# Kernel optimization log

Measured on AMD Instinct MI355X. Metric: run time of the kernel, lower is better.

## Reference

```python
import jax, jax.numpy as jnp
import numpy as np

DEL_ID, STOP_ID, PAD_ID, KEEP_ID = 3, 5, 0, 2


def lstm(x, h0, c0, Wi, Wh, bi, bh):
    """Single-layer batch-first LSTM, PyTorch gate order (i,f,g,o).
    x: [B,T,E]; h0,c0: [B,H]. Returns (ys [B,T,H], h [B,H], c [B,H])."""
    b = bi + bh

    def step(carry, xt):
        h, c = carry
        g = xt @ Wi.T + h @ Wh.T + b  # [B,4H]
        i, f, gg, o = jnp.split(g, 4, axis=-1)
        c = jax.nn.sigmoid(f) * c + jax.nn.sigmoid(i) * jnp.tanh(gg)
        h = jax.nn.sigmoid(o) * jnp.tanh(c)
        return (h, c), h

    (h, c), ys = jax.lax.scan(step, (h0, c0), jnp.swapaxes(x, 0, 1))
    return jnp.swapaxes(ys, 0, 1), h, c


def setup_inputs() -> dict:
    key = jax.random.key(0)
    ks = jax.random.split(key, 20)
    B, T, S, H, E, V = 32, 100, 100, 512, 256, 30000
    s = 0.02
    inp = {
        "input_edits": jax.random.randint(ks[0], (B, T), 0, V),
        "simp_sent": jax.random.randint(ks[1], (B, S), 0, V),
        "org_ids": jax.random.randint(ks[2], (B, S), 0, V),
        "encoder_outputs_org": jax.random.normal(ks[3], (B, S, H), dtype=jnp.float32),
        "h0": jnp.zeros((B, H), jnp.float32),
        "c0": jnp.zeros((B, H), jnp.float32),
        "emb": jax.random.normal(ks[4], (V, E), dtype=jnp.float32) * s,
        "Wi_e": jax.random.normal(ks[5], (4 * H, E), dtype=jnp.float32) * s,
        "Wh_e": jax.random.normal(ks[6], (4 * H, H), dtype=jnp.float32) * s,
        "bi_e": jnp.zeros((4 * H,), jnp.float32),
        "bh_e": jnp.zeros((4 * H,), jnp.float32),
        "Wi_w": jax.random.normal(ks[7], (4 * H, E), dtype=jnp.float32) * s,
        "Wh_w": jax.random.normal(ks[8], (4 * H, H), dtype=jnp.float32) * s,
        "bi_w": jnp.zeros((4 * H,), jnp.float32),
        "bh_w": jnp.zeros((4 * H,), jnp.float32),
        "Wp": jax.random.normal(ks[9], (H, H), dtype=jnp.float32) * s,
        "Wm": jax.random.normal(ks[10], (E, 4 * H), dtype=jnp.float32) * s,
        "bm": jnp.zeros((E,), jnp.float32),
        "b_out": jnp.zeros((30000,), jnp.float32),
    }
    return inp


def reference(input_edits, simp_sent, org_ids, encoder_outputs_org, h0, c0,
              emb, Wi_e, Wh_e, bi_e, bh_e, Wi_w, Wh_w, bi_w, bh_w,
              Wp, Wm, bm, b_out):
    # teacher_forcing_ratio = 1.0 -> teacher-forcing branch only
    B, T = input_edits.shape
    S = encoder_outputs_org.shape[1]
    Sw = simp_sent.shape[1]

    # run both LSTMs over the full teacher-forced sequences
    out_e, he, ce = lstm(emb[input_edits], h0, c0, Wi_e, Wh_e, bi_e, bh_e)  # [B,T,H]
    out_w, _, _ = lstm(emb[simp_sent], h0, c0, Wi_w, Wh_w, bi_w, bh_w)      # [B,Sw,H]

    # attention over encoder outputs
    key_org = out_e @ Wp.T                                                   # [B,T,H]
    attn = jax.nn.softmax(jnp.einsum('bth,bsh->bts', key_org, encoder_outputs_org), axis=-1)
    applied = jnp.einsum('bts,bsh->bth', attn, encoder_outputs_org)          # [B,T,H]

    # counters are exclusive cumsums of gold-action masks over input_edits[:,1:]
    a = input_edits[:, 1:]                                                   # gold actions, [B,T-1]
    inc_del = ((a == KEEP_ID) | (a == DEL_ID)).astype(jnp.int32)
    inc_ins = ((a != DEL_ID) & (a != STOP_ID) & (a != PAD_ID)).astype(jnp.int32)
    ctr_del = jnp.clip(jnp.cumsum(inc_del, 1) - inc_del, 0, S - 1)           # [B,T-1]
    ctr_ins = jnp.clip(jnp.cumsum(inc_ins, 1) - inc_ins, 0, Sw - 1)

    H = encoder_outputs_org.shape[2]
    c = jnp.take_along_axis(encoder_outputs_org,
                            jnp.broadcast_to(ctr_del[:, :, None], (B, T - 1, H)), axis=1)
    c_word = jnp.take_along_axis(out_w,
                                 jnp.broadcast_to(ctr_ins[:, :, None], (B, T - 1, H)), axis=1)

    feat = jnp.concatenate([out_e[:, :T - 1], applied[:, :T - 1], c, c_word], axis=-1)  # [B,T-1,4H]
    hmlp = jnp.tanh(feat @ Wm.T + bm)                                        # [B,T-1,E]
    logp = jax.nn.log_softmax(hmlp @ emb.T + b_out, axis=-1)                 # [B,T-1,V]
    return logp, he[None], ce[None]
```

## Files before the change

kernel.cpp:

```cpp
#include <hip/hip_runtime.h>
#include <math.h>


typedef __attribute__((ext_vector_type(8))) short short8v;
typedef __attribute__((ext_vector_type(4))) float f32x4;
typedef unsigned long long ull;

#define LSTM_BLOCKS 64
#define NTIL 235

__device__ __forceinline__ float sigf(float x){ return 1.0f/(1.0f + __expf(-x)); }
__device__ __forceinline__ float tanhc(float x){
  x = fminf(fmaxf(x, -15.f), 15.f);
  float e = __expf(2.f*x);
  return (e-1.f)/(e+1.f);
}
__device__ __forceinline__ short f2bf(float f){
  unsigned u = __float_as_uint(f);
  u = (u + 0x7fffu + ((u >> 16) & 1u)) >> 16;
  return (short)u;
}
__device__ __forceinline__ float bf2f(short s){
  return __uint_as_float(((unsigned)(unsigned short)s) << 16);
}

__global__ void prep_permute(
    const float* __restrict__ Wi_e, const float* __restrict__ Wh_e,
    const float* __restrict__ bi_e, const float* __restrict__ bh_e,
    const float* __restrict__ Wi_w, const float* __restrict__ Wh_w,
    const float* __restrict__ bi_w, const float* __restrict__ bh_w,
    short* __restrict__ WiPh_e, short* __restrict__ WhPh_e, float* __restrict__ biasP_e,
    short* __restrict__ WiPh_w, short* __restrict__ WhPh_w, float* __restrict__ biasP_w)
{
  const int z = blockIdx.y;
  const float* Wi = z ? Wi_w : Wi_e;
  const float* Wh = z ? Wh_w : Wh_e;
  const float* bi = z ? bi_w : bi_e;
  const float* bh = z ? bh_w : bh_e;
  short* WiPh = z ? WiPh_w : WiPh_e;
  short* WhPh = z ? WhPh_w : WhPh_e;
  float* biasP = z ? biasP_w : biasP_e;

  int idx = blockIdx.x*256 + threadIdx.x;
  {
    int op = idx >> 9, k = idx & 511;
    int u = op >> 2, g = op & 3;
    WhPh[idx] = f2bf(Wh[(g*512+u)*512 + k]);
  }
  if (idx < 2048*256) {
    int op = idx >> 8, e = idx & 255;
    int u = op >> 2, g = op & 3;
    WiPh[idx] = f2bf(Wi[(g*512+u)*256 + e]);
  }
  if (idx < 2048) {
    int u = idx >> 2, g = idx & 3;
    biasP[idx] = bi[g*512+u] + bh[g*512+u];
  }
}

__global__ void misc_prep(const float* __restrict__ emb,
                          const float* __restrict__ Wp, const float* __restrict__ Wm,
                          const float* __restrict__ h0, const int* __restrict__ ie,
                          short* __restrict__ embh,
                          short* __restrict__ Wph, short* __restrict__ Wmh,
                          ull* __restrict__ hq, unsigned* __restrict__ bar,
                          int* __restrict__ ctr_del, int* __restrict__ ctr_ins)
{
  int idx = blockIdx.x*256 + threadIdx.x;
  if (idx < 1920000) {
    float4 v = *(const float4*)(emb + (long)idx*4);
    short4 o; o.x=f2bf(v.x); o.y=f2bf(v.y); o.z=f2bf(v.z); o.w=f2bf(v.w);
    *(short4*)(embh + (long)idx*4) = o;
  } else if (idx < 1985536) {
    int i = idx - 1920000;
    float4 v = *(const float4*)(Wp + (long)i*4);
    short4 o; o.x=f2bf(v.x); o.y=f2bf(v.y); o.z=f2bf(v.z); o.w=f2bf(v.w);
    *(short4*)(Wph + (long)i*4) = o;
  } else if (idx < 2116608) {
    int i = idx - 1985536;
    float4 v = *(const float4*)(Wm + (long)i*4);
    short4 o; o.x=f2bf(v.x); o.y=f2bf(v.y); o.z=f2bf(v.z); o.w=f2bf(v.w);
    *(short4*)(Wmh + (long)i*4) = o;
  } else if (idx < 2124800) {
    int i = idx - 2116608;
    int b = (i >> 7) & 31, q = i & 127;
    const float* src = h0 + b*512 + q*4;
    ull v = ((ull)(unsigned short)f2bf(src[3]) << 48) |
            ((ull)(unsigned short)f2bf(src[2]) << 32) |
            ((ull)(unsigned short)f2bf(src[1]) << 16) |
            ((ull)(unsigned short)f2bf(src[0]));
    hq[i] = v;
  } else if (idx < 2124928) {
    bar[idx - 2124800] = 0u;
  } else if (idx < 2124960) {
    int b = idx - 2124928;
    int rd = 0, ri = 0;
    for (int t = 0; t < 99; ++t) {
      int a = ie[b*100 + t + 1];
      int incd = (a == 2 || a == 3) ? 1 : 0;
      int inci = (a != 3 && a != 5 && a != 0) ? 1 : 0;
      ctr_del[b*99 + t] = min(rd, 99);
      ctr_ins[b*99 + t] = min(ri, 99);
      rd += incd; ri += inci;
    }
  }
}

__global__ __launch_bounds__(256) void enc_prep(const float* __restrict__ enc,
                                                short* __restrict__ ench,
                                                short* __restrict__ encTh)
{
  __shared__ short tile[100][72];
  const int b = blockIdx.x;
  const float* src = enc + (long)b*51200;
  short* de = ench  + (long)b*51200;
  short* dt = encTh + (long)b*65536;
  const int tid = threadIdx.x;
  for (int c = 0; c < 8; ++c) {
    #pragma unroll
    for (int i = 0; i < 25; ++i) {
      int idx = tid + 256*i;
      int k = idx >> 6, j = idx & 63;
      short h = f2bf(src[(long)k*512 + c*64 + j]);
      tile[k][j] = h;
      de[(long)k*512 + c*64 + j] = h;
    }
    __syncthreads();
    #pragma unroll
    for (int i = 0; i < 32; ++i) {
      int idx = tid + 256*i;
      int n = idx >> 7, kk = idx & 127;
      dt[(long)(c*64 + n)*128 + kk] = (kk < 100) ? tile[kk][n] : (short)0;
    }
    __syncthreads();
  }
}

template<int GATHER,int CVT_A,int BIAS,int TANH,int OUT_BF16>
__device__ __forceinline__ void gemm_mfma_body(
    const void* __restrict__ Av, const int* __restrict__ tok,
    const short* __restrict__ Bh, const float* __restrict__ bias,
    void* __restrict__ Cv, int M, int N, int K, int lda, int ldc,
    int bxk, int byk)
{
  __shared__ short As[128][72];
  __shared__ short Bs[128][72];
  const int bm = bxk * 128;
  const int bn = byk * 128;
  const int tid = threadIdx.x;
  const int w = tid >> 6, l = tid & 63;
  const int wr = (w >> 1) * 64, wc = (w & 1) * 64;
  const int lr = l & 15, kg = l >> 4;

  f32x4 acc[4][4] = {};

  for (int k0 = 0; k0 < K; k0 += 64) {
    #pragma unroll
    for (int q = 0; q < 4; ++q) {
      int ci = tid + 256*q;
      int r = ci >> 3, ch = ci & 7;
      int ar = bm + r; if (ar > M-1) ar = M-1;
      if (GATHER) ar = tok[ar];
      if (CVT_A) {
        const float* ap = ((const float*)Av) + (long)ar*lda + k0 + ch*8;
        float4 v0 = *(const float4*)ap;
        float4 v1 = *(const float4*)(ap + 4);
        short8v s;
        s[0]=f2bf(v0.x); s[1]=f2bf(v0.y); s[2]=f2bf(v0.z); s[3]=f2bf(v0.w);
        s[4]=f2bf(v1.x); s[5]=f2bf(v1.y); s[6]=f2bf(v1.z); s[7]=f2bf(v1.w);
        *(short8v*)&As[r][ch*8] = s;
      } else {
        *(short8v*)&As[r][ch*8] =
            *(const short8v*)(((const short*)Av) + (long)ar*lda + k0 + ch*8);
      }
      int br = bn + r; if (br > N-1) br = N-1;
      *(short8v*)&Bs[r][ch*8] = *(const short8v*)(Bh + (long)br*K + k0 + ch*8);
    }
    __syncthreads();
    #pragma unroll
    for (int ks = 0; ks < 2; ++ks) {
      short8v a[4], b[4];
      #pragma unroll
      for (int m = 0; m < 4; ++m)
        a[m] = *(const short8v*)&As[wr + m*16 + lr][ks*32 + kg*8];
      #pragma unroll
      for (int n = 0; n < 4; ++n)
        b[n] = *(const short8v*)&Bs[wc + n*16 + lr][ks*32 + kg*8];
      #pragma unroll
      for (int m = 0; m < 4; ++m)
        #pragma unroll
        for (int n = 0; n < 4; ++n)
          acc[m][n] = __builtin_amdgcn_mfma_f32_16x16x32_bf16(a[m], b[n], acc[m][n], 0, 0, 0);
    }
    __syncthreads();
  }

  #pragma unroll
  for (int n = 0; n < 4; ++n) {
    int col = bn + wc + n*16 + lr;
    bool cok = (col < N);
    float bv = (BIAS && cok) ? bias[col] : 0.f;
    #pragma unroll
    for (int m = 0; m < 4; ++m) {
      int row0 = bm + wr + m*16 + kg*4;
      #pragma unroll
      for (int r = 0; r < 4; ++r) {
        int row = row0 + r;
        if (cok && row < M) {
          float v = acc[m][n][r] + bv;
          if (TANH) v = tanhc(v);
          if (OUT_BF16) ((short*)Cv)[(long)row*ldc + col] = f2bf(v);
          else          ((float*)Cv)[(long)row*ldc + col] = v;
        }
      }
    }
  }
}

template<int GATHER,int CVT_A,int BIAS,int TANH,int OUT_BF16>
__global__ __launch_bounds__(256) void gemm_mfma(
    const void* __restrict__ Av, const int* __restrict__ tok,
    const short* __restrict__ Bh, const float* __restrict__ bias,
    void* __restrict__ Cv, int M, int N, int K, int lda, int ldc)
{
  gemm_mfma_body<GATHER,CVT_A,BIAS,TANH,OUT_BF16>(
      Av, tok, Bh, bias, Cv, M, N, K, lda, ldc, blockIdx.x, blockIdx.y);
}

template<int BIAS,int TANH,int OUT_BF16>
__global__ __launch_bounds__(256) void gemm_mfma_bat(
    const short* __restrict__ Ah, const short* __restrict__ Bh,
    const float* __restrict__ bias, void* __restrict__ Cv,
    int M, int N, int K, int lda, int ldc, long sA, long sB, long sC)
{
  const int z = blockIdx.z;
  void* C2 = OUT_BF16 ? (void*)((short*)Cv + (long)z*sC)
                      : (void*)((float*)Cv + (long)z*sC);
  gemm_mfma_body<0,0,BIAS,TANH,OUT_BF16>(
      (const void*)(Ah + (long)z*sA), nullptr, Bh + (long)z*sB, bias,
      C2, M, N, K, lda, ldc, blockIdx.x, blockIdx.y);
}

__global__ __launch_bounds__(256) void xproj_mfma(
    const float* __restrict__ emb,
    const int* __restrict__ tokA, const int* __restrict__ tokB,
    const short* __restrict__ WA, const short* __restrict__ WB,
    const float* __restrict__ bA, const float* __restrict__ bB,
    short* __restrict__ outA, short* __restrict__ outB)
{
  const int z = blockIdx.z;
  gemm_mfma_body<1,1,1,0,1>(
      emb, z ? tokB : tokA, z ? WB : WA, z ? bB : bA,
      z ? (void*)outB : (void*)outA, 3200, 2048, 256, 256, 2048,
      blockIdx.x, blockIdx.y);
}

__global__ __launch_bounds__(256) void logits_mfma_partial(
    const short* __restrict__ Ah,
    const short* __restrict__ Bh,
    const float* __restrict__ bias,
    short* __restrict__ Cg,
    float2* __restrict__ partial)
{
  __shared__ short As[128][72];
  __shared__ short Bs[128][72];
  __shared__ float2 red[128][2];
  const int bm = blockIdx.x * 128;
  const int bn = blockIdx.y * 128;
  const int tid = threadIdx.x;
  const int w = tid >> 6, l = tid & 63;
  const int wr = (w >> 1) * 64, wc = (w & 1) * 64;
  const int lr = l & 15, kg = l >> 4;

  f32x4 acc[4][4] = {};

  #pragma unroll
  for (int k0 = 0; k0 < 256; k0 += 64) {
    #pragma unroll
    for (int q = 0; q < 4; ++q) {
      int ci = tid + 256*q;
      int r = ci >> 3, ch = ci & 7;
      int ar = bm + r; if (ar > 3167) ar = 3167;
      *(short8v*)&As[r][ch*8] = *(const short8v*)(Ah + (long)ar*256 + k0 + ch*8);
      int br = bn + r; if (br > 29999) br = 29999;
      *(short8v*)&Bs[r][ch*8] = *(const short8v*)(Bh + (long)br*256 + k0 + ch*8);
    }
    __syncthreads();
    #pragma unroll
    for (int ks = 0; ks < 2; ++ks) {
      short8v a[4], b[4];
      #pragma unroll
      for (int m = 0; m < 4; ++m)
        a[m] = *(const short8v*)&As[wr + m*16 + lr][ks*32 + kg*8];
      #pragma unroll
      for (int n = 0; n < 4; ++n)
        b[n] = *(const short8v*)&Bs[wc + n*16 + lr][ks*32 + kg*8];
      #pragma unroll
      for (int m = 0; m < 4; ++m)
        #pragma unroll
        for (int n = 0; n < 4; ++n)
          acc[m][n] = __builtin_amdgcn_mfma_f32_16x16x32_bf16(a[m], b[n], acc[m][n], 0, 0, 0);
    }
    __syncthreads();
  }

  #pragma unroll
  for (int n = 0; n < 4; ++n) {
    int col = bn + wc + n*16 + lr;
    float bv = (col < 30000) ? bias[col] : 0.f;
    #pragma unroll
    for (int m = 0; m < 4; ++m)
      #pragma unroll
      for (int r = 0; r < 4; ++r)
        acc[m][n][r] = (col < 30000) ? acc[m][n][r] + bv : -INFINITY;
  }
  #pragma unroll
  for (int m = 0; m < 4; ++m) {
    #pragma unroll
    for (int r = 0; r < 4; ++r) {
      float a0 = acc[m][0][r], a1 = acc[m][1][r], a2 = acc[m][2][r], a3 = acc[m][3][r];
      float mx = fmaxf(fmaxf(a0, a1), fmaxf(a2, a3));
      #pragma unroll
      for (int off = 1; off < 16; off <<= 1) mx = fmaxf(mx, __shfl_xor(mx, off));
      float se = 0.f;
      if (mx > -INFINITY)
        se = __expf(a0-mx) + __expf(a1-mx) + __expf(a2-mx) + __expf(a3-mx);
      #pragma unroll
      for (int off = 1; off < 16; off <<= 1) se += __shfl_xor(se, off);
      if (lr == 0) red[wr + m*16 + kg*4 + r][w & 1] = make_float2(mx, se);
    }
  }
  #pragma unroll
  for (int n = 0; n < 4; ++n) {
    int col = bn + wc + n*16 + lr;
    if (col < 30000) {
      #pragma unroll
      for (int m = 0; m < 4; ++m) {
        int row0 = bm + wr + m*16 + kg*4;
        #pragma unroll
        for (int r = 0; r < 4; ++r) {
          int row = row0 + r;
          if (row < 3168) Cg[(long)row*30000 + col] = f2bf(acc[m][n][r]);
        }
      }
    }
  }
  __syncthreads();
  if (tid < 128) {
    int row = bm + tid;
    if (row < 3168) {
      float2 A = red[tid][0], B = red[tid][1];
      float M = fmaxf(A.x, B.x);
      float S = 0.f;
      if (M > -INFINITY) S = A.y*__expf(A.x - M) + B.y*__expf(B.x - M);
      partial[(long)row*NTIL + blockIdx.y] = make_float2(M, S);
    }
  }
}

__global__ __launch_bounds__(256) void sub_lse_fused(
    const short* __restrict__ Cg, const float2* __restrict__ partial,
    float* __restrict__ out)
{
  int row = blockIdx.x;
  int tid = threadIdx.x;
  float m = -INFINITY, s = 0.f;
  if (tid < NTIL) {
    float2 p = partial[(long)row*NTIL + tid];
    m = p.x; s = p.y;
  }
  #pragma unroll
  for (int off = 32; off; off >>= 1) {
    float om = __shfl_xor(m, off);
    float os = __shfl_xor(s, off);
    float nm = fmaxf(m, om);
    if (nm > -INFINITY) {
      s = s*__expf(m - nm) + os*__expf(om - nm);
      m = nm;
    }
  }
  __shared__ float sm[4], ss[4], lsh;
  int wv = tid >> 6;
  if ((tid & 63) == 0) { sm[wv] = m; ss[wv] = s; }
  __syncthreads();
  if (tid == 0) {
    float M = sm[0], S = ss[0];
    #pragma unroll
    for (int i = 1; i < 4; ++i) {
      float nm = fmaxf(M, sm[i]);
      S = S*__expf(M - nm) + ss[i]*__expf(sm[i] - nm);
      M = nm;
    }
    lsh = M + __logf(S);
  }
  __syncthreads();
  float lv = lsh;
  const short* src = Cg + (long)row*30000;
  float* dst = out + (long)row*30000;
  for (int i = tid; i < 3750; i += 256) {
    short8v v = *(const short8v*)(src + i*8);
    float4 o0, o1;
    o0.x = bf2f(v[0]) - lv; o0.y = bf2f(v[1]) - lv;
    o0.z = bf2f(v[2]) - lv; o0.w = bf2f(v[3]) - lv;
    o1.x = bf2f(v[4]) - lv; o1.y = bf2f(v[5]) - lv;
    o1.z = bf2f(v[6]) - lv; o1.w = bf2f(v[7]) - lv;
    *(float4*)(dst + i*8)     = o0;
    *(float4*)(dst + i*8 + 4) = o1;
  }
}

__global__ __launch_bounds__(256, 1) void lstm_persist(
    const short* __restrict__ WhPh_e, const short* __restrict__ WhPh_w,
    const short* __restrict__ Xp_e, const short* __restrict__ Xp_w,
    const float* __restrict__ c0_in,
    ull* __restrict__ hq,
    short* __restrict__ outT,
    float* __restrict__ out_hc,
    unsigned* __restrict__ flags)
{
  const int bx = blockIdx.x;
  const int l = bx >> 5;
  const int ublk = bx & 31;
  const int tid = threadIdx.x;
  const int w = tid >> 6, lane = tid & 63;
  const int uloc = lane >> 4;
  const int bn = lane & 15;
  const int u_global = ublk*16 + w*4 + uloc;
  const int ob = (ublk*16 + w*4) * 4;
  const int qcol = ublk*4 + w;

  const short* WhPh = l ? WhPh_w : WhPh_e;
  const short* Xp   = l ? Xp_w   : Xp_e;
  const unsigned* myfl = flags + l*32;

  __shared__ short hT[32][520];

  __hip_atomic_load(&flags[100], __ATOMIC_ACQUIRE, __HIP_MEMORY_SCOPE_AGENT);

  short8v afr[16];
  {
    const short* wp = WhPh + (long)(ob + bn)*512 + uloc*8;
    #pragma unroll
    for (int ks = 0; ks < 16; ++ks)
      afr[ks] = *(const short8v*)(wp + ks*32);
  }
  float c_s0 = c0_in[bn*512 + u_global];
  float c_s1 = c0_in[(bn+16)*512 + u_global];

  for (int t = 0; t < 100; ++t) {
    ull xq0 = *(const ull*)(Xp + ((long)(bn*100 + t))*2048 + u_global*4);
    ull xq1 = *(const ull*)(Xp + ((long)((bn+16)*100 + t))*2048 + u_global*4);
    if (t) {
      int ok;
      do {
        unsigned f = (lane < 32)
          ? __hip_atomic_load(&myfl[lane], __ATOMIC_RELAXED, __HIP_MEMORY_SCOPE_AGENT)
          : 0xffffffffu;
        ok = __all((int)(f >= (unsigned)t));
        if (!ok) __builtin_amdgcn_s_sleep(1);
      } while (!ok);
    }
    {
      const ull* hsrc = hq + (size_t)t*8192 + (l << 12);
      #pragma unroll
      for (int i = 0; i < 16; ++i) {
        int idx = tid + 256*i;
        int b = idx >> 7, q = idx & 127;
        *(ull*)&hT[b][q*4] = hsrc[idx];
      }
    }
    __syncthreads();
    f32x4 acc0 = {}, acc1 = {};
    #pragma unroll
    for (int ks = 0; ks < 16; ++ks) {
      short8v b0 = *(const short8v*)&hT[bn][ks*32 + uloc*8];
      short8v b1 = *(const short8v*)&hT[bn+16][ks*32 + uloc*8];
      acc0 = __builtin_amdgcn_mfma_f32_16x16x32_bf16(afr[ks], b0, acc0, 0, 0, 0);
      acc1 = __builtin_amdgcn_mfma_f32_16x16x32_bf16(afr[ks], b1, acc1, 0, 0, 0);
    }
    float gi = acc0[0] + bf2f((short)(xq0 & 0xffffu));
    float gf = acc0[1] + bf2f((short)((xq0 >> 16) & 0xffffu));
    float gg = acc0[2] + bf2f((short)((xq0 >> 32) & 0xffffu));
    float go = acc0[3] + bf2f((short)((xq0 >> 48) & 0xffffu));
    c_s0 = sigf(gf)*c_s0 + sigf(gi)*tanhc(gg);
    float hv0 = sigf(go)*tanhc(c_s0);
    gi = acc1[0] + bf2f((short)(xq1 & 0xffffu));
    gf = acc1[1] + bf2f((short)((xq1 >> 16) & 0xffffu));
    gg = acc1[2] + bf2f((short)((xq1 >> 32) & 0xffffu));
    go = acc1[3] + bf2f((short)((xq1 >> 48) & 0xffffu));
    c_s1 = sigf(gf)*c_s1 + sigf(gi)*tanhc(gg);
    float hv1 = sigf(go)*tanhc(c_s1);

    short hb0 = f2bf(hv0), hb1 = f2bf(hv1);
    unsigned p0 = (unsigned)(unsigned short)hb0;
    unsigned p1 = (unsigned)(unsigned short)hb1;
    unsigned a1 = __shfl_down((int)p0, 16), a2 = __shfl_down((int)p0, 32), a3 = __shfl_down((int)p0, 48);
    unsigned e1 = __shfl_down((int)p1, 16), e2 = __shfl_down((int)p1, 32), e3 = __shfl_down((int)p1, 48);
    if (uloc == 0) {
      ull q0 = ((ull)((a2 & 0xffffu) | (a3 << 16)) << 32) | ((p0 & 0xffffu) | (a1 << 16));
      ull q1 = ((ull)((e2 & 0xffffu) | (e3 << 16)) << 32) | ((p1 & 0xffffu) | (e1 << 16));
      ull* hd = hq + (size_t)(t+1)*8192 + (l << 12);
      __hip_atomic_store(&hd[(bn << 7) + qcol],      q0, __ATOMIC_RELAXED, __HIP_MEMORY_SCOPE_AGENT);
      __hip_atomic_store(&hd[((bn+16) << 7) + qcol], q1, __ATOMIC_RELAXED, __HIP_MEMORY_SCOPE_AGENT);
    }
    if (t < 99) {
      asm volatile("s_waitcnt vmcnt(0)" ::: "memory");
      __syncthreads();
      if (tid == 0)
        __hip_atomic_store(&flags[bx], (unsigned)(t+1),
                           __ATOMIC_RELAXED, __HIP_MEMORY_SCOPE_AGENT);
    }
    short* od = outT + ((long)(l*100 + t)*512 + u_global)*32;
    od[bn]    = hb0;
    od[bn+16] = hb1;
    if (t == 99 && l == 0) {
      out_hc[bn*512 + u_global]              = hv0;
      out_hc[(bn+16)*512 + u_global]         = hv1;
      out_hc[16384 + bn*512 + u_global]      = c_s0;
      out_hc[16384 + (bn+16)*512 + u_global] = c_s1;
    }
  }
}

__global__ __launch_bounds__(256) void transpose_out(
    const short* __restrict__ outT, short* __restrict__ out_e, short* __restrict__ out_w)
{
  __shared__ short tile[512][40];
  const int t = blockIdx.x, l = blockIdx.y;
  const short* src = outT + (long)(l*100 + t)*16384;
  const int tid = threadIdx.x;
  #pragma unroll
  for (int i = 0; i < 8; ++i) {
    int fi = tid + 256*i;
    int u = fi >> 2, b8 = (fi & 3)*8;
    *(short8v*)&tile[u][b8] = *(const short8v*)(src + fi*8);
  }
  __syncthreads();
  short* dst = l ? out_w : out_e;
  for (int b = 0; b < 32; ++b) {
    short* drow = dst + (long)(b*100 + t)*512;
    drow[tid]     = tile[tid][b];
    drow[tid+256] = tile[tid+256][b];
  }
}

__global__ void softmax_rows(const float* __restrict__ P, short* __restrict__ Ph)
{
  int row  = blockIdx.x*4 + (threadIdx.x >> 6);
  int lane = threadIdx.x & 63;
  const float* p = P + (long)row*128;
  short* q = Ph + (long)row*128;
  float x0 = p[lane];
  float x1 = (lane + 64 < 100) ? p[lane+64] : -INFINITY;
  float m = fmaxf(x0, x1);
  #pragma unroll
  for (int off = 32; off; off >>= 1) m = fmaxf(m, __shfl_xor(m, off));
  float e0 = __expf(x0 - m);
  float e1 = (lane + 64 < 100) ? __expf(x1 - m) : 0.f;
  float s = e0 + e1;
  #pragma unroll
  for (int off = 32; off; off >>= 1) s += __shfl_xor(s, off);
  float inv = 1.f / s;
  q[lane]      = f2bf(e0 * inv);
  q[lane + 64] = (lane + 64 < 100) ? f2bf(e1 * inv) : (short)0;
}

__global__ void feat_kernel(const short* __restrict__ out_e, const short* __restrict__ appliedh,
                            const short* __restrict__ ench, const short* __restrict__ out_w,
                            const int* __restrict__ ctr_del, const int* __restrict__ ctr_ins,
                            short* __restrict__ feat)
{
  int n = blockIdx.x;
  int b = n / 99, t = n % 99;
  int tid = threadIdx.x;
  int seg = tid >> 6;
  int off = (tid & 63) * 8;
  const short* s = (seg == 0) ? out_e    + (long)(b*100 + t)*512
                 : (seg == 1) ? appliedh + (long)(b*100 + t)*512
                 : (seg == 2) ? ench     + (long)(b*100 + ctr_del[n])*512
                              : out_w    + (long)(b*100 + ctr_ins[n])*512;
  *(short8v*)(feat + (long)n*2048 + seg*512 + off) = *(const short8v*)(s + off);
}

extern "C" void kernel_launch(void* const* d_in, const int* in_sizes, int n_in,
                              void* d_out, int out_size, void* d_ws, size_t ws_size,
                              hipStream_t stream)
{
  const int*   input_edits = (const int*)  d_in[0];
  const int*   simp_sent   = (const int*)  d_in[1];
  const float* enc   = (const float*)d_in[3];
  const float* h0    = (const float*)d_in[4];
  const float* c0    = (const float*)d_in[5];
  const float* emb   = (const float*)d_in[6];
  const float* Wi_e  = (const float*)d_in[7];
  const float* Wh_e  = (const float*)d_in[8];
  const float* bi_e  = (const float*)d_in[9];
  const float* bh_e  = (const float*)d_in[10];
  const float* Wi_w  = (const float*)d_in[11];
  const float* Wh_w  = (const float*)d_in[12];
  const float* bi_w  = (const float*)d_in[13];
  const float* bh_w  = (const float*)d_in[14];
  const float* Wp    = (const float*)d_in[15];
  const float* Wm    = (const float*)d_in[16];
  const float* bmv   = (const float*)d_in[17];
  const float* b_out = (const float*)d_in[18];
  float* out = (float*)d_out;

  float* ws = (float*)d_ws;
  size_t off = 0;
  auto alloc = [&](size_t n){ float* p = ws + off; off += (n + 63) & ~(size_t)63; return p; };

  short* WiPh_e   = (short*)alloc(262144);
  short* WiPh_w   = (short*)alloc(262144);
  float* biasP_e  = alloc(2048);
  float* biasP_w  = alloc(2048);
  short* WhPh_e   = (short*)alloc(524288);
  short* WhPh_w   = (short*)alloc(524288);
  short* Xp_e     = (short*)alloc(3276800);
  short* Xp_w     = (short*)alloc(3276800);
  short* outT     = (short*)alloc(1638400);
  short* out_e    = (short*)alloc(819200);
  short* out_w    = (short*)alloc(819200);
  ull*   hq       = (ull*)alloc(101*8192*2);
  unsigned* bar   = (unsigned*)alloc(128);
  float* Pbuf     = alloc(409600);
  short* Pbh      = (short*)alloc(204800);
  int*   ctr_del  = (int*)alloc(3168);
  int*   ctr_ins  = (int*)alloc(3168);
  short* Wph      = (short*)alloc(131072);
  short* Wmh      = (short*)alloc(262144);
  short* keyh     = (short*)alloc(819200);
  short* appliedh = (short*)alloc(819200);
  short* ench     = (short*)alloc(819200);
  short* encTh    = (short*)alloc(1048576);
  short* embh     = (short*)alloc(3840000);
  short* logith   = (short*)alloc(47520000);
  float2* partial = (float2*)alloc(3168*NTIL*2);
  short* feath    = (short*)Xp_e;
  short* hmlph    = (short*)Xp_w;

  prep_permute<<<dim3(4096,2), 256, 0, stream>>>(
      Wi_e, Wh_e, bi_e, bh_e, Wi_w, Wh_w, bi_w, bh_w,
      WiPh_e, WhPh_e, biasP_e, WiPh_w, WhPh_w, biasP_w);
  misc_prep<<<8301, 256, 0, stream>>>(emb, Wp, Wm, h0, input_edits,
                                      embh, Wph, Wmh, hq, bar, ctr_del, ctr_ins);
  enc_prep<<<32, 256, 0, stream>>>(enc, ench, encTh);

  xproj_mfma<<<dim3(25,16,2), 256, 0, stream>>>(
      emb, input_edits, simp_sent, WiPh_e, WiPh_w, biasP_e, biasP_w, Xp_e, Xp_w);

  lstm_persist<<<LSTM_BLOCKS, 256, 0, stream>>>(
      WhPh_e, WhPh_w, Xp_e, Xp_w, c0, hq, outT, out + 95040000L, bar);

  transpose_out<<<dim3(100,2), 256, 0, stream>>>(outT, out_e, out_w);

  gemm_mfma<0,0,0,0,1><<<dim3(25,4), 256, 0, stream>>>(
      out_e, nullptr, Wph, nullptr, keyh, 3200, 512, 512, 512, 512);

  gemm_mfma_bat<0,0,0><<<dim3(1,1,32), 256, 0, stream>>>(
      keyh, ench, nullptr, Pbuf, 100, 100, 512, 512, 128,
      51200, 51200, 12800);
  softmax_rows<<<800, 256, 0, stream>>>(Pbuf, Pbh);
  gemm_mfma_bat<0,0,1><<<dim3(1,4,32), 256, 0, stream>>>(
      Pbh, encTh, nullptr, appliedh, 100, 512, 128, 128, 512,
      12800, 65536, 51200);

  feat_kernel<<<3168, 256, 0, stream>>>(out_e, appliedh, ench, out_w,
                                        ctr_del, ctr_ins, feath);
  gemm_mfma<0,0,1,1,1><<<dim3(25,2), 256, 0, stream>>>(
      feath, nullptr, Wmh, bmv, hmlph, 3168, 256, 2048, 2048, 256);

  logits_mfma_partial<<<dim3(25, NTIL), 256, 0, stream>>>(
      hmlph, embh, b_out, logith, partial);
  sub_lse_fused<<<3168, 256, 0, stream>>>(logith, partial, out);
}
```

Baseline: 1.056 ms.

## Use per-wave padded flags in LSTM and derive outputs from hq history

Result: no change. 1.076 ms (+1.9%).

```diff
diff --git a/kernel.cpp b/kernel.cpp
--- a/kernel.cpp
+++ b/kernel.cpp
@@ -63,7 +63,7 @@
                           const float* __restrict__ h0, const int* __restrict__ ie,
                           short* __restrict__ embh,
                           short* __restrict__ Wph, short* __restrict__ Wmh,
-                          ull* __restrict__ hq, unsigned* __restrict__ bar,
+                          ull* __restrict__ hq, unsigned* __restrict__ flags,
                           int* __restrict__ ctr_del, int* __restrict__ ctr_ins)
 {
   int idx = blockIdx.x*256 + threadIdx.x;
@@ -90,10 +90,10 @@
             ((ull)(unsigned short)f2bf(src[1]) << 16) |
             ((ull)(unsigned short)f2bf(src[0]));
     hq[i] = v;
-  } else if (idx < 2124928) {
-    bar[idx - 2124800] = 0u;
-  } else if (idx < 2124960) {
-    int b = idx - 2124928;
+  } else if (idx < 2128960) {
+    flags[idx - 2124800] = 0u;
+  } else if (idx < 2128992) {
+    int b = idx - 2128960;
     int rd = 0, ri = 0;
     for (int t = 0; t < 99; ++t) {
       int a = ie[b*100 + t + 1];
@@ -414,7 +414,6 @@
     const short* __restrict__ Xp_e, const short* __restrict__ Xp_w,
     const float* __restrict__ c0_in,
     ull* __restrict__ hq,
-    short* __restrict__ outT,
     float* __restrict__ out_hc,
     unsigned* __restrict__ flags)
 {
@@ -428,14 +427,15 @@
   const int u_global = ublk*16 + w*4 + uloc;
   const int ob = (ublk*16 + w*4) * 4;
   const int qcol = ublk*4 + w;
+  const int fidx = (l*128 + ublk*4 + w) * 16;
 
   const short* WhPh = l ? WhPh_w : WhPh_e;
   const short* Xp   = l ? Xp_w   : Xp_e;
-  const unsigned* myfl = flags + l*32;
+  const unsigned* flb = flags + l*2048;
 
   __shared__ short hT[32][520];
 
-  __hip_atomic_load(&flags[100], __ATOMIC_ACQUIRE, __HIP_MEMORY_SCOPE_AGENT);
+  __hip_atomic_load(&flags[4096], __ATOMIC_ACQUIRE, __HIP_MEMORY_SCOPE_AGENT);
 
   short8v afr[16];
   {
@@ -450,16 +450,18 @@
   for (int t = 0; t < 100; ++t) {
     ull xq0 = *(const ull*)(Xp + ((long)(bn*100 + t))*2048 + u_global*4);
     ull xq1 = *(const ull*)(Xp + ((long)((bn+16)*100 + t))*2048 + u_global*4);
-    if (t) {
+    if (t && w == 0) {
       int ok;
       do {
-        unsigned f = (lane < 32)
-          ? __hip_atomic_load(&myfl[lane], __ATOMIC_RELAXED, __HIP_MEMORY_SCOPE_AGENT)
-          : 0xffffffffu;
-        ok = __all((int)(f >= (unsigned)t));
+        unsigned f0 = __hip_atomic_load(flb + lane*16,
+                         __ATOMIC_RELAXED, __HIP_MEMORY_SCOPE_AGENT);
+        unsigned f1 = __hip_atomic_load(flb + (lane + 64)*16,
+                         __ATOMIC_RELAXED, __HIP_MEMORY_SCOPE_AGENT);
+        ok = __all(f0 >= (unsigned)t && f1 >= (unsigned)t);
         if (!ok) __builtin_amdgcn_s_sleep(1);
       } while (!ok);
     }
+    __syncthreads();
     {
       const ull* hsrc = hq + (size_t)t*8192 + (l << 12);
       #pragma unroll
@@ -505,14 +507,10 @@
     }
     if (t < 99) {
       asm volatile("s_waitcnt vmcnt(0)" ::: "memory");
-      __syncthreads();
-      if (tid == 0)
-        __hip_atomic_store(&flags[bx], (unsigned)(t+1),
+      if (lane == 0)
+        __hip_atomic_store(&flags[fidx], (unsigned)(t+1),
                            __ATOMIC_RELAXED, __HIP_MEMORY_SCOPE_AGENT);
     }
-    short* od = outT + ((long)(l*100 + t)*512 + u_global)*32;
-    od[bn]    = hb0;
-    od[bn+16] = hb1;
     if (t == 99 && l == 0) {
       out_hc[bn*512 + u_global]              = hv0;
       out_hc[(bn+16)*512 + u_global]         = hv1;
@@ -522,25 +520,18 @@
   }
 }
 
-__global__ __launch_bounds__(256) void transpose_out(
-    const short* __restrict__ outT, short* __restrict__ out_e, short* __restrict__ out_w)
-{
-  __shared__ short tile[512][40];
+__global__ __launch_bounds__(256) void copy_out(
+    const ull* __restrict__ hq, short* __restrict__ out_e, short* __restrict__ out_w)
+{
   const int t = blockIdx.x, l = blockIdx.y;
-  const short* src = outT + (long)(l*100 + t)*16384;
+  const ull* src = hq + (size_t)(t+1)*8192 + (l << 12);
+  short* dst = l ? out_w : out_e;
   const int tid = threadIdx.x;
   #pragma unroll
-  for (int i = 0; i < 8; ++i) {
-    int fi = tid + 256*i;
-    int u = fi >> 2, b8 = (fi & 3)*8;
-    *(short8v*)&tile[u][b8] = *(const short8v*)(src + fi*8);
-  }
-  __syncthreads();
-  short* dst = l ? out_w : out_e;
-  for (int b = 0; b < 32; ++b) {
-    short* drow = dst + (long)(b*100 + t)*512;
-    drow[tid]     = tile[tid][b];
-    drow[tid+256] = tile[tid+256][b];
+  for (int i = 0; i < 16; ++i) {
+    int idx = tid + 256*i;
+    int b = idx >> 7, q = idx & 127;
+    ((ull*)(dst + (long)(b*100 + t)*512))[q] = src[idx];
   }
 }
 
@@ -618,11 +609,10 @@
   short* WhPh_w   = (short*)alloc(524288);
   short* Xp_e     = (short*)alloc(3276800);
   short* Xp_w     = (short*)alloc(3276800);
-  short* outT     = (short*)alloc(1638400);
   short* out_e    = (short*)alloc(819200);
   short* out_w    = (short*)alloc(819200);
   ull*   hq       = (ull*)alloc(101*8192*2);
-  unsigned* bar   = (unsigned*)alloc(128);
+  unsigned* flags = (unsigned*)alloc(4224);
   float* Pbuf     = alloc(409600);
   short* Pbh      = (short*)alloc(204800);
   int*   ctr_del  = (int*)alloc(3168);
@@ -642,17 +632,17 @@
   prep_permute<<<dim3(4096,2), 256, 0, stream>>>(
       Wi_e, Wh_e, bi_e, bh_e, Wi_w, Wh_w, bi_w, bh_w,
       WiPh_e, WhPh_e, biasP_e, WiPh_w, WhPh_w, biasP_w);
-  misc_prep<<<8301, 256, 0, stream>>>(emb, Wp, Wm, h0, input_edits,
-                                      embh, Wph, Wmh, hq, bar, ctr_del, ctr_ins);
+  misc_prep<<<8317, 256, 0, stream>>>(emb, Wp, Wm, h0, input_edits,
+                                      embh, Wph, Wmh, hq, flags, ctr_del, ctr_ins);
   enc_prep<<<32, 256, 0, stream>>>(enc, ench, encTh);
 
   xproj_mfma<<<dim3(25,16,2), 256, 0, stream>>>(
       emb, input_edits, simp_sent, WiPh_e, WiPh_w, biasP_e, biasP_w, Xp_e, Xp_w);
 
   lstm_persist<<<LSTM_BLOCKS, 256, 0, stream>>>(
-      WhPh_e, WhPh_w, Xp_e, Xp_w, c0, hq, outT, out + 95040000L, bar);
-
-  transpose_out<<<dim3(100,2), 256, 0, stream>>>(outT, out_e, out_w);
+      WhPh_e, WhPh_w, Xp_e, Xp_w, c0, hq, out + 95040000L, flags);
+
+  copy_out<<<dim3(100,2), 256, 0, stream>>>(hq, out_e, out_w);
 
   gemm_mfma<0,0,0,0,1><<<dim3(25,4), 256, 0, stream>>>(
       out_e, nullptr, Wph, nullptr, keyh, 3200, 512, 512, 512, 512);
```
